# Performance work log

Hardware: AMD Instinct MI355X
Metric: run time of the kernel (lower is better)

The kernel has to match this reference:

```python
import jax, jax.numpy as jnp
import numpy as np

N_NODES, N_EDGES, H = 25000, 400000, 64
EPS = 1e-15


def _norm(x):
    return jnp.sqrt(jnp.sum(x * x, axis=-1, keepdims=True))


def _projx(x, c):
    norm = _norm(x)
    max_norm = (1.0 - 1e-5) / jnp.sqrt(c)
    scale = jnp.minimum(max_norm / jnp.maximum(norm, EPS), 1.0)
    return x * scale


def _expmap0(x, c):
    norm = _norm(x)
    sc = jnp.sqrt(c)
    return jnp.tanh(sc * norm) * x / (norm * sc + EPS)


def _logmap0(x, c):
    norm = _norm(x)
    sc = jnp.sqrt(c)
    return (1.0 / sc) * jnp.arctanh(jnp.minimum(sc * norm, 1.0 - 1e-5)) * x / (norm + EPS)


def _mobius_add(x, y, c):
    x2 = jnp.sum(x * x, axis=-1, keepdims=True)
    y2 = jnp.sum(y * y, axis=-1, keepdims=True)
    xy = jnp.sum(x * y, axis=-1, keepdims=True)
    num = (1.0 + 2.0 * c * xy + c * y2) * x + (1.0 - c * x2) * y
    denom = 1.0 + 2.0 * c * xy + c * c * x2 * y2
    return num / (denom + EPS)


def _mobius_linear(x, W, b, c):
    t = _logmap0(x, c)
    out = t @ W.T + b
    return _expmap0(out, c)


def setup_inputs() -> dict:
    key = jax.random.key(0)
    ks = jax.random.split(key, 12)
    h_V = jax.random.normal(ks[0], (N_NODES, H), dtype=jnp.float32) * 0.3
    h_E = jax.random.normal(ks[1], (N_EDGES, 3 * H), dtype=jnp.float32) * 0.3
    src = jax.random.randint(ks[2], (N_EDGES,), 0, N_NODES, dtype=jnp.int32)
    dst = jax.random.randint(ks[3], (N_EDGES,), 0, N_NODES, dtype=jnp.int32)
    log_c = jnp.zeros((), dtype=jnp.float32)  # c = 1.0

    def lin(k, out_d, in_d):
        bound = 1.0 / np.sqrt(in_d)
        kw, kb = jax.random.split(k)
        W = jax.random.uniform(kw, (out_d, in_d), jnp.float32, -bound, bound)
        b = jax.random.uniform(kb, (out_d,), jnp.float32, -bound, bound)
        return W, b

    W1_w, W1_b = lin(ks[4], H, 5 * H)
    W2_w, W2_b = lin(ks[5], H, H)
    W3_w, W3_b = lin(ks[6], H, H)
    return {"h_V": h_V, "h_E": h_E, "src": src, "dst": dst, "log_c": log_c,
            "W1_w": W1_w, "W1_b": W1_b, "W2_w": W2_w, "W2_b": W2_b,
            "W3_w": W3_w, "W3_b": W3_b}


def reference(h_V, h_E, src, dst, log_c, W1_w, W1_b, W2_w, W2_b, W3_w, W3_b):
    c = jnp.exp(log_c)
    n_nodes = h_V.shape[0]
    h_E = _projx(h_E, c)
    h_V = _projx(h_V, c)
    # edge gather -> fused mobius-linear chain  [E, 5H] -> [E, H]
    h_EV = jnp.concatenate([h_E, h_V[src], h_V[dst]], axis=-1)
    h_EV = _mobius_linear(h_EV, W1_w, W1_b, c)
    h_EV = _mobius_linear(_projx(jax.nn.relu(h_EV), c), W2_w, W2_b, c)
    h_msg = _mobius_linear(_projx(jax.nn.relu(h_EV), c), W3_w, W3_b, c)
    # hyperbolic aggregate: logmap0 -> scatter-mean over src -> expmap0
    tangent = _logmap0(h_msg, c)
    sums = jax.ops.segment_sum(tangent, src, num_segments=n_nodes)
    counts = jax.ops.segment_sum(jnp.ones((tangent.shape[0],), tangent.dtype), src,
                                 num_segments=n_nodes)
    agg_t = sums / jnp.maximum(counts, 1.0)[:, None]
    agg = _expmap0(agg_t, c)
    h_V = _mobius_add(h_V, agg, c)  # dropout disabled (eval)
    return _projx(h_V, c)
```

## Files before the change

### kernel.cpp

```cpp
#include <hip/hip_runtime.h>
#include <hip/hip_bf16.h>
#include <math.h>

#define EPSF 1e-15f

typedef __attribute__((ext_vector_type(8))) short bf16x8;
typedef __attribute__((ext_vector_type(16))) float f32x16;

__device__ __forceinline__ unsigned short f2bf(float x) {
    unsigned u = __float_as_uint(x);
    u += 0x7fffu + ((u >> 16) & 1u);
    return (unsigned short)(u >> 16);
}
__device__ __forceinline__ float bf2f(unsigned short b) {
    return __uint_as_float(((unsigned)b) << 16);
}
__device__ __forceinline__ unsigned pkbf(float lo, float hi) {
    __hip_bfloat162 h = __float22bfloat162_rn(make_float2(lo, hi));
    return *reinterpret_cast<unsigned*>(&h);
}
__device__ __forceinline__ float fast_tanh_pos(float x) {
    if (x < 0.25f) { float x2 = x * x; return x * (1.0f - x2 * (0.33333334f - 0.13333334f * x2)); }
    float e = __expf(2.0f * x);
    return 1.0f - 2.0f / (e + 1.0f);
}
__device__ __forceinline__ float fast_atanh01(float y) {
    if (y < 0.125f) { float y2 = y * y; return y * (1.0f + y2 * (0.33333334f + 0.2f * y2)); }
    return 0.5f * __logf((1.0f + y) / (1.0f - y));
}

__device__ __forceinline__ float wred(float v) {
#pragma unroll
    for (int off = 32; off; off >>= 1) v += __shfl_xor(v, off);
    return v;
}

__global__ void prep_wfrag(const float* __restrict__ W1, const float* __restrict__ W2,
                           const float* __restrict__ W3, unsigned short* __restrict__ Wf) {
    int idx = blockIdx.x * blockDim.x + threadIdx.x;
    if (idx >= 56 * 64) return;
    int fid = idx >> 6, lane = idx & 63;
    int e31 = lane & 31, hi = lane >> 5;
    unsigned short* dstp = Wf + ((size_t)fid * 64 + lane) * 8;
    if (fid < 40) {
        int ks = fid >> 1, t = fid & 1;
        int n = 32 * t + e31;
        int k0 = 16 * ks + 8 * hi;
#pragma unroll
        for (int i = 0; i < 8; ++i) dstp[i] = f2bf(W1[n * 320 + k0 + i]);
    } else {
        const float* srcW = (fid < 48) ? W2 : W3;
        int b = (fid < 48) ? fid - 40 : fid - 48;
        int ks = b >> 1, t2 = b & 1;
        int n = 32 * t2 + e31;
        int cb = 32 * (ks >> 1) + 16 * (ks & 1) + 4 * hi;
#pragma unroll
        for (int i = 0; i < 8; ++i) dstp[i] = f2bf(srcW[n * 64 + cb + 8 * (i >> 2) + (i & 3)]);
    }
}

__global__ void __launch_bounds__(256)
node_prep(const float* __restrict__ hV, const float* __restrict__ logc,
          unsigned short* __restrict__ hVp, float* __restrict__ pj, int n_nodes) {
    int wid  = (blockIdx.x * blockDim.x + threadIdx.x) >> 6;
    int lane = threadIdx.x & 63;
    if (wid >= n_nodes) return;
    float c    = __expf(logc[0]);
    float scq  = sqrtf(c);
    float maxn = (1.0f - 1e-5f) / scq;
    float x = hV[(size_t)wid * 64 + lane];
    float p = wred(x * x);
    float sS = fminf(maxn / fmaxf(sqrtf(p), EPSF), 1.0f);
    hVp[(size_t)wid * 64 + lane] = f2bf(x * sS);
    if (lane == 0) pj[wid] = sS * sS * p;
}

__global__ void hist_kernel(const int* __restrict__ src, int* __restrict__ cnt,
                            int* __restrict__ slot, int n_edges) {
    int e = blockIdx.x * blockDim.x + threadIdx.x;
    if (e < n_edges) slot[e] = atomicAdd(&cnt[src[e]], 1);
}

__global__ void __launch_bounds__(1024)
scan_rowptr(const int* __restrict__ cnt, int* __restrict__ rowptr, int n) {
    __shared__ int wpart[16];
    int C   = (n + 1023) >> 10;
    int tid = threadIdx.x;
    int beg = tid * C;
    int end = beg + C; if (end > n) end = n;
    int s = 0;
    if (beg < n) for (int k = beg; k < end; ++k) s += cnt[k];
    int lane = tid & 63, wv = tid >> 6;
    int v = s;
#pragma unroll
    for (int off = 1; off < 64; off <<= 1) {
        int t = __shfl_up(v, off);
        if (lane >= off) v += t;
    }
    if (lane == 63) wpart[wv] = v;
    __syncthreads();
    if (tid < 64) {
        int t = (tid < 16) ? wpart[tid] : 0;
#pragma unroll
        for (int off = 1; off < 16; off <<= 1) {
            int u = __shfl_up(t, off);
            if (lane >= off) t += u;
        }
        if (tid < 16) wpart[tid] = t;
    }
    __syncthreads();
    int base = (wv ? wpart[wv - 1] : 0) + (v - s);
    if (beg < n) {
        int run = base;
        for (int k = beg; k < end; ++k) { rowptr[k] = run; run += cnt[k]; }
    }
    if (tid == 1023) rowptr[n] = wpart[15];
}

__global__ void slotfix_kernel(const int* __restrict__ src, const int* __restrict__ rowptr,
                               int* __restrict__ slot, int n_edges) {
    int e = blockIdx.x * blockDim.x + threadIdx.x;
    if (e < n_edges) slot[e] += rowptr[src[e]];
}

__device__ __forceinline__ void stage_mlp32(float (&v)[2][16],
                                            const bf16x8* __restrict__ Wfrag, int fbase,
                                            const float* __restrict__ bvec,
                                            float scq, float maxn, int lane, int hi) {
    float n2 = 0.f, rn2 = 0.f;
    float u[2][16];
#pragma unroll
    for (int t = 0; t < 2; ++t)
#pragma unroll
        for (int j = 0; j < 16; ++j) {
            float x = v[t][j];
            n2 = fmaf(x, x, n2);
            float y = fmaxf(x, 0.f);
            u[t][j] = y;
            rn2 = fmaf(y, y, rn2);
        }
    n2  += __shfl_xor(n2, 32);
    rn2 += __shfl_xor(rn2, 32);
    float n  = sqrtf(n2);
    float h  = fast_tanh_pos(scq * n) / (n * scq + EPSF);
    float rn = h * sqrtf(rn2);
    float ps = fminf(maxn / fmaxf(rn, EPSF), 1.0f);
    float pn = rn * ps;
    float gg = fast_atanh01(fminf(scq * pn, 1.0f - 1e-5f)) / (scq * (pn + EPSF));
    float f2 = h * ps * gg;

    f32x16 acc[2] = {};
#pragma unroll
    for (int ks = 0; ks < 4; ++ks) {
        int t = ks >> 1, jb = 8 * (ks & 1);
        union { bf16x8 b; unsigned w[4]; } B;
        B.w[0] = pkbf(u[t][jb + 0], u[t][jb + 1]);
        B.w[1] = pkbf(u[t][jb + 2], u[t][jb + 3]);
        B.w[2] = pkbf(u[t][jb + 4], u[t][jb + 5]);
        B.w[3] = pkbf(u[t][jb + 6], u[t][jb + 7]);
#pragma unroll
        for (int t2 = 0; t2 < 2; ++t2)
            acc[t2] = __builtin_amdgcn_mfma_f32_32x32x16_bf16(
                Wfrag[(size_t)(fbase + ks * 2 + t2) * 64 + lane], B.b, acc[t2], 0, 0, 0);
    }
#pragma unroll
    for (int t2 = 0; t2 < 2; ++t2)
#pragma unroll
        for (int q = 0; q < 4; ++q) {
            const float4 bv = *reinterpret_cast<const float4*>(&bvec[32 * t2 + 8 * q + 4 * hi]);
            v[t2][4 * q + 0] = fmaf(f2, acc[t2][4 * q + 0], bv.x);
            v[t2][4 * q + 1] = fmaf(f2, acc[t2][4 * q + 1], bv.y);
            v[t2][4 * q + 2] = fmaf(f2, acc[t2][4 * q + 2], bv.z);
            v[t2][4 * q + 3] = fmaf(f2, acc[t2][4 * q + 3], bv.w);
        }
}

__global__ void __launch_bounds__(256)
edge_mfma(const float* __restrict__ hE, const int* __restrict__ src,
          const int* __restrict__ dst, const float* __restrict__ logc,
          const unsigned short* __restrict__ Wf, const unsigned short* __restrict__ hVp,
          const float* __restrict__ pj,
          const float* __restrict__ b1, const float* __restrict__ b2,
          const float* __restrict__ b3, const int* __restrict__ slot,
          unsigned short* __restrict__ tg, int n_edges) {
    int lane = threadIdx.x & 63;
    int w    = threadIdx.x >> 6;
    int tile = blockIdx.x * 4 + w;
    int e0 = tile * 32;
    if (e0 >= n_edges) return;

    float c    = __expf(logc[0]);
    float scq  = sqrtf(c);
    float maxn = (1.0f - 1e-5f) / scq;

    int e31 = lane & 31, hi = lane >> 5;
    int ev = e0 + e31; if (ev >= n_edges) ev = n_edges - 1;
    int s16 = src[ev], d16 = dst[ev];
    float pjS = pj[s16], pjD = pj[d16];

    const bf16x8* Wfrag = reinterpret_cast<const bf16x8*>(Wf);

    const bf16x8* vsp = reinterpret_cast<const bf16x8*>(hVp + (size_t)s16 * 64);
    const bf16x8* vdp = reinterpret_cast<const bf16x8*>(hVp + (size_t)d16 * 64);
    bf16x8 aS[4], aD[4];
#pragma unroll
    for (int q = 0; q < 4; ++q) { aS[q] = vsp[2 * q + hi]; aD[q] = vdp[2 * q + hi]; }

    f32x16 accE[2] = {}, accV[2] = {};
    float pE = 0.f;
    const float* eb = hE + (size_t)ev * 192 + 8 * hi;
#pragma unroll
    for (int ks = 0; ks < 12; ++ks) {
        const float4* p4 = reinterpret_cast<const float4*>(eb + 16 * ks);
        float4 a0 = p4[0], a1 = p4[1];
        pE += a0.x*a0.x + a0.y*a0.y + a0.z*a0.z + a0.w*a0.w
            + a1.x*a1.x + a1.y*a1.y + a1.z*a1.z + a1.w*a1.w;
        union { bf16x8 b; unsigned u[4]; } cv;
        cv.u[0] = pkbf(a0.x, a0.y);
        cv.u[1] = pkbf(a0.z, a0.w);
        cv.u[2] = pkbf(a1.x, a1.y);
        cv.u[3] = pkbf(a1.z, a1.w);
#pragma unroll
        for (int t = 0; t < 2; ++t)
            accE[t] = __builtin_amdgcn_mfma_f32_32x32x16_bf16(
                Wfrag[(size_t)(ks * 2 + t) * 64 + lane], cv.b, accE[t], 0, 0, 0);
    }
#pragma unroll
    for (int q = 0; q < 4; ++q) {
#pragma unroll
        for (int t = 0; t < 2; ++t)
            accV[t] = __builtin_amdgcn_mfma_f32_32x32x16_bf16(
                Wfrag[(size_t)((12 + q) * 2 + t) * 64 + lane], aS[q], accV[t], 0, 0, 0);
    }
#pragma unroll
    for (int q = 0; q < 4; ++q) {
#pragma unroll
        for (int t = 0; t < 2; ++t)
            accV[t] = __builtin_amdgcn_mfma_f32_32x32x16_bf16(
                Wfrag[(size_t)((16 + q) * 2 + t) * 64 + lane], aD[q], accV[t], 0, 0, 0);
    }

    pE += __shfl_xor(pE, 32);
    float sE = fminf(maxn / fmaxf(sqrtf(pE), EPSF), 1.0f);
    float nt = sqrtf(sE * sE * pE + pjS + pjD);
    float gq = fast_atanh01(fminf(scq * nt, 1.0f - 1e-5f)) / (scq * (nt + EPSF));

    float v[2][16];
#pragma unroll
    for (int t = 0; t < 2; ++t)
#pragma unroll
        for (int q = 0; q < 4; ++q) {
            const float4 bv = *reinterpret_cast<const float4*>(&b1[32 * t + 8 * q + 4 * hi]);
            v[t][4*q+0] = fmaf(gq, fmaf(sE, accE[t][4*q+0], accV[t][4*q+0]), bv.x);
            v[t][4*q+1] = fmaf(gq, fmaf(sE, accE[t][4*q+1], accV[t][4*q+1]), bv.y);
            v[t][4*q+2] = fmaf(gq, fmaf(sE, accE[t][4*q+2], accV[t][4*q+2]), bv.z);
            v[t][4*q+3] = fmaf(gq, fmaf(sE, accE[t][4*q+3], accV[t][4*q+3]), bv.w);
        }

    stage_mlp32(v, Wfrag, 40, b2, scq, maxn, lane, hi);
    stage_mlp32(v, Wfrag, 48, b3, scq, maxn, lane, hi);

    float n2 = 0.f;
#pragma unroll
    for (int t = 0; t < 2; ++t)
#pragma unroll
        for (int j = 0; j < 16; ++j) n2 = fmaf(v[t][j], v[t][j], n2);
    n2 += __shfl_xor(n2, 32);
    float n  = sqrtf(n2);
    float h  = fast_tanh_pos(scq * n) / (n * scq + EPSF);
    float hn = h * n;
    float g4 = fast_atanh01(fminf(scq * hn, 1.0f - 1e-5f)) / (scq * (hn + EPSF));
    float fT = g4 * h;

    if (e0 + e31 < n_edges) {
        int sl = slot[ev];
        unsigned short* orow = tg + (size_t)sl * 64;
#pragma unroll
        for (int t = 0; t < 2; ++t)
#pragma unroll
            for (int q = 0; q < 4; ++q) {
                uint2 o;
                o.x = pkbf(fT * v[t][4*q+0], fT * v[t][4*q+1]);
                o.y = pkbf(fT * v[t][4*q+2], fT * v[t][4*q+3]);
                *reinterpret_cast<uint2*>(&orow[32 * t + 8 * q + 4 * hi]) = o;
            }
    }
}

__global__ void __launch_bounds__(256)
node_gather(const float* __restrict__ hV, const float* __restrict__ logc,
            const unsigned short* __restrict__ tg, const int* __restrict__ rowptr,
            float* __restrict__ out, int n_nodes) {
    int wid  = (blockIdx.x * blockDim.x + threadIdx.x) >> 6;
    int lane = threadIdx.x & 63;
    if (wid >= n_nodes) return;

    float c    = __expf(logc[0]);
    float scq  = sqrtf(c);
    float maxn = (1.0f - 1e-5f) / scq;

    int beg = rowptr[wid], end = rowptr[wid + 1];
    int g = lane >> 4, i15 = lane & 15;
    float s0 = 0.f, s1 = 0.f, s2 = 0.f, s3 = 0.f;
    for (int i = beg + g; i < end; i += 4) {
        uint2 p = *reinterpret_cast<const uint2*>(&tg[(size_t)i * 64 + i15 * 4]);
        s0 += bf2f((unsigned short)(p.x & 0xffff));
        s1 += bf2f((unsigned short)(p.x >> 16));
        s2 += bf2f((unsigned short)(p.y & 0xffff));
        s3 += bf2f((unsigned short)(p.y >> 16));
    }
    s0 += __shfl_xor(s0, 16); s0 += __shfl_xor(s0, 32);
    s1 += __shfl_xor(s1, 16); s1 += __shfl_xor(s1, 32);
    s2 += __shfl_xor(s2, 16); s2 += __shfl_xor(s2, 32);
    s3 += __shfl_xor(s3, 16); s3 += __shfl_xor(s3, 32);
    int srcl = lane >> 2;
    float a0 = __shfl(s0, srcl), a1 = __shfl(s1, srcl);
    float a2 = __shfl(s2, srcl), a3 = __shfl(s3, srcl);
    float ssum = (lane & 2) ? ((lane & 1) ? a3 : a2) : ((lane & 1) ? a1 : a0);

    float inv = 1.f / fmaxf((float)(end - beg), 1.f);
    float at  = ssum * inv;

    float an2 = wred(at * at);
    float an  = sqrtf(an2);
    float ae  = fast_tanh_pos(scq * an) / (an * scq + EPSF);

    float xv  = hV[(size_t)wid * 64 + lane];
    float hs2 = wred(xv * xv);
    float sX  = fminf(maxn / fmaxf(sqrtf(hs2), EPSF), 1.0f);

    float x = sX * xv, y = ae * at;
    float x2 = wred(x * x);
    float y2 = wred(y * y);
    float xy = wred(x * y);

    float ca = 1.f + 2.f * c * xy + c * y2;
    float cb = 1.f - c * x2;
    float id = 1.f / (1.f + 2.f * c * xy + c * c * x2 * y2 + EPSF);

    float r   = (ca * x + cb * y) * id;
    float rn2 = wred(r * r);
    float rs  = fminf(maxn / fmaxf(sqrtf(rn2), EPSF), 1.0f);

    out[(size_t)wid * 64 + lane] = rs * r;
}

extern "C" void kernel_launch(void* const* d_in, const int* in_sizes, int n_in,
                              void* d_out, int out_size, void* d_ws, size_t ws_size,
                              hipStream_t stream) {
    const float* hV   = (const float*)d_in[0];
    const float* hE   = (const float*)d_in[1];
    const int*   src  = (const int*)d_in[2];
    const int*   dst  = (const int*)d_in[3];
    const float* logc = (const float*)d_in[4];
    const float* W1   = (const float*)d_in[5];
    const float* b1   = (const float*)d_in[6];
    const float* W2   = (const float*)d_in[7];
    const float* b2   = (const float*)d_in[8];
    const float* W3   = (const float*)d_in[9];
    const float* b3   = (const float*)d_in[10];

    int n_nodes = in_sizes[0] / 64;
    int n_edges = in_sizes[2];
    float* out = (float*)d_out;

    char* wsb = (char*)d_ws;
    unsigned short* Wf = (unsigned short*)wsb;
    size_t off = 56 * 512 * sizeof(unsigned short);
    int* cnt    = (int*)(wsb + off);   off += (size_t)n_nodes * 4;
    int* rowptr = (int*)(wsb + off);   off += (size_t)(n_nodes + 1) * 4;
    int* slot   = (int*)(wsb + off);   off += (size_t)n_edges * 4;
    float* pj   = (float*)(wsb + off); off += (size_t)n_nodes * 4;
    off = (off + 15) & ~(size_t)15;
    unsigned short* hVp = (unsigned short*)(wsb + off);
    off += (size_t)n_nodes * 64 * 2;
    off = (off + 15) & ~(size_t)15;
    unsigned short* tg = (unsigned short*)(wsb + off);

    hipMemsetAsync(cnt, 0, (size_t)n_nodes * sizeof(int), stream);

    prep_wfrag<<<(56 * 64 + 255) / 256, 256, 0, stream>>>(W1, W2, W3, Wf);
    node_prep<<<(n_nodes + 3) / 4, 256, 0, stream>>>(hV, logc, hVp, pj, n_nodes);
    hist_kernel<<<(n_edges + 255) / 256, 256, 0, stream>>>(src, cnt, slot, n_edges);
    scan_rowptr<<<1, 1024, 0, stream>>>(cnt, rowptr, n_nodes);
    slotfix_kernel<<<(n_edges + 255) / 256, 256, 0, stream>>>(src, rowptr, slot, n_edges);

    int tiles = (n_edges + 31) / 32;
    edge_mfma<<<(tiles + 3) / 4, 256, 0, stream>>>(
        hE, src, dst, logc, Wf, hVp, pj, b1, b2, b3, slot, tg, n_edges);

    node_gather<<<(n_nodes + 3) / 4, 256, 0, stream>>>(
        hV, logc, tg, rowptr, out, n_nodes);
}
```

Before: 242.3 us.

## Stage MFMA weight fragments in LDS and prefetch edge features into registers

Each block copies the full bf16 weight fragment array (56 KB) into shared memory and the MFMA loops read weights from LDS instead of global/L1. All edge-feature float4 loads and the slot index are now issued up front, before the MFMA chain, so their memory latency can overlap. Launch bounds now request 2 blocks per SM. The trade-off is a 56 KB per-block LDS fill plus a barrier on every block, lower occupancy from the LDS footprint, and extra register pressure from the 24 prefetched float4 values.

Result: faster. 220.9 us (-8.8%).

```diff
diff --git a/kernel.cpp b/kernel.cpp
--- a/kernel.cpp
+++ b/kernel.cpp
@@ -124,7 +124,7 @@
 }
 
 __device__ __forceinline__ void stage_mlp32(float (&v)[2][16],
-                                            const bf16x8* __restrict__ Wfrag, int fbase,
+                                            const unsigned short* WfL, int fbase,
                                             const float* __restrict__ bvec,
                                             float scq, float maxn, int lane, int hi) {
     float n2 = 0.f, rn2 = 0.f;
@@ -159,9 +159,11 @@
         B.w[2] = pkbf(u[t][jb + 4], u[t][jb + 5]);
         B.w[3] = pkbf(u[t][jb + 6], u[t][jb + 7]);
 #pragma unroll
-        for (int t2 = 0; t2 < 2; ++t2)
-            acc[t2] = __builtin_amdgcn_mfma_f32_32x32x16_bf16(
-                Wfrag[(size_t)(fbase + ks * 2 + t2) * 64 + lane], B.b, acc[t2], 0, 0, 0);
+        for (int t2 = 0; t2 < 2; ++t2) {
+            bf16x8 wf = *reinterpret_cast<const bf16x8*>(
+                &WfL[((fbase + ks * 2 + t2) * 64 + lane) * 8]);
+            acc[t2] = __builtin_amdgcn_mfma_f32_32x32x16_bf16(wf, B.b, acc[t2], 0, 0, 0);
+        }
     }
 #pragma unroll
     for (int t2 = 0; t2 < 2; ++t2)
@@ -175,7 +177,7 @@
         }
 }
 
-__global__ void __launch_bounds__(256)
+__global__ void __launch_bounds__(256, 2)
 edge_mfma(const float* __restrict__ hE, const int* __restrict__ src,
           const int* __restrict__ dst, const float* __restrict__ logc,
           const unsigned short* __restrict__ Wf, const unsigned short* __restrict__ hVp,
@@ -183,6 +185,16 @@
           const float* __restrict__ b1, const float* __restrict__ b2,
           const float* __restrict__ b3, const int* __restrict__ slot,
           unsigned short* __restrict__ tg, int n_edges) {
+    __shared__ __align__(16) unsigned short WfL[28672];
+    {
+        const uint4* wsrc = reinterpret_cast<const uint4*>(Wf);
+        uint4* wdst = reinterpret_cast<uint4*>(WfL);
+#pragma unroll
+        for (int i = 0; i < 14; ++i)
+            wdst[i * 256 + threadIdx.x] = wsrc[i * 256 + threadIdx.x];
+    }
+    __syncthreads();
+
     int lane = threadIdx.x & 63;
     int w    = threadIdx.x >> 6;
     int tile = blockIdx.x * 4 + w;
@@ -197,9 +209,16 @@
     int ev = e0 + e31; if (ev >= n_edges) ev = n_edges - 1;
     int s16 = src[ev], d16 = dst[ev];
     float pjS = pj[s16], pjD = pj[d16];
-
-    const bf16x8* Wfrag = reinterpret_cast<const bf16x8*>(Wf);
-
+    int sl = slot[ev];
+
+    float4 ha[24];
+    const float* eb = hE + (size_t)ev * 192 + 8 * hi;
+#pragma unroll
+    for (int ks = 0; ks < 12; ++ks) {
+        const float4* p4 = reinterpret_cast<const float4*>(eb + 16 * ks);
+        ha[2 * ks]     = p4[0];
+        ha[2 * ks + 1] = p4[1];
+    }
     const bf16x8* vsp = reinterpret_cast<const bf16x8*>(hVp + (size_t)s16 * 64);
     const bf16x8* vdp = reinterpret_cast<const bf16x8*>(hVp + (size_t)d16 * 64);
     bf16x8 aS[4], aD[4];
@@ -208,11 +227,9 @@
 
     f32x16 accE[2] = {}, accV[2] = {};
     float pE = 0.f;
-    const float* eb = hE + (size_t)ev * 192 + 8 * hi;
 #pragma unroll
     for (int ks = 0; ks < 12; ++ks) {
-        const float4* p4 = reinterpret_cast<const float4*>(eb + 16 * ks);
-        float4 a0 = p4[0], a1 = p4[1];
+        float4 a0 = ha[2 * ks], a1 = ha[2 * ks + 1];
         pE += a0.x*a0.x + a0.y*a0.y + a0.z*a0.z + a0.w*a0.w
             + a1.x*a1.x + a1.y*a1.y + a1.z*a1.z + a1.w*a1.w;
         union { bf16x8 b; unsigned u[4]; } cv;
@@ -221,23 +238,26 @@
         cv.u[2] = pkbf(a1.x, a1.y);
         cv.u[3] = pkbf(a1.z, a1.w);
 #pragma unroll
-        for (int t = 0; t < 2; ++t)
-            accE[t] = __builtin_amdgcn_mfma_f32_32x32x16_bf16(
-                Wfrag[(size_t)(ks * 2 + t) * 64 + lane], cv.b, accE[t], 0, 0, 0);
+        for (int t = 0; t < 2; ++t) {
+            bf16x8 wf = *reinterpret_cast<const bf16x8*>(&WfL[((ks * 2 + t) * 64 + lane) * 8]);
+            accE[t] = __builtin_amdgcn_mfma_f32_32x32x16_bf16(wf, cv.b, accE[t], 0, 0, 0);
+        }
     }
 #pragma unroll
     for (int q = 0; q < 4; ++q) {
 #pragma unroll
-        for (int t = 0; t < 2; ++t)
-            accV[t] = __builtin_amdgcn_mfma_f32_32x32x16_bf16(
-                Wfrag[(size_t)((12 + q) * 2 + t) * 64 + lane], aS[q], accV[t], 0, 0, 0);
+        for (int t = 0; t < 2; ++t) {
+            bf16x8 wf = *reinterpret_cast<const bf16x8*>(&WfL[(((12 + q) * 2 + t) * 64 + lane) * 8]);
+            accV[t] = __builtin_amdgcn_mfma_f32_32x32x16_bf16(wf, aS[q], accV[t], 0, 0, 0);
+        }
     }
 #pragma unroll
     for (int q = 0; q < 4; ++q) {
 #pragma unroll
-        for (int t = 0; t < 2; ++t)
-            accV[t] = __builtin_amdgcn_mfma_f32_32x32x16_bf16(
-                Wfrag[(size_t)((16 + q) * 2 + t) * 64 + lane], aD[q], accV[t], 0, 0, 0);
+        for (int t = 0; t < 2; ++t) {
+            bf16x8 wf = *reinterpret_cast<const bf16x8*>(&WfL[(((16 + q) * 2 + t) * 64 + lane) * 8]);
+            accV[t] = __builtin_amdgcn_mfma_f32_32x32x16_bf16(wf, aD[q], accV[t], 0, 0, 0);
+        }
     }
 
     pE += __shfl_xor(pE, 32);
@@ -257,8 +277,8 @@
             v[t][4*q+3] = fmaf(gq, fmaf(sE, accE[t][4*q+3], accV[t][4*q+3]), bv.w);
         }
 
-    stage_mlp32(v, Wfrag, 40, b2, scq, maxn, lane, hi);
-    stage_mlp32(v, Wfrag, 48, b3, scq, maxn, lane, hi);
+    stage_mlp32(v, WfL, 40, b2, scq, maxn, lane, hi);
+    stage_mlp32(v, WfL, 48, b3, scq, maxn, lane, hi);
 
     float n2 = 0.f;
 #pragma unroll
@@ -273,7 +293,6 @@
     float fT = g4 * h;
 
     if (e0 + e31 < n_edges) {
-        int sl = slot[ev];
         unsigned short* orow = tg + (size_t)sl * 64;
 #pragma unroll
         for (int t = 0; t < 2; ++t)
```
